# Kernel optimization log

Measured on AMD Instinct MI355X. Metric: run time of the kernel, lower is better.

## Reference

```python
import jax, jax.numpy as jnp
import numpy as np

HIDDEN = 1024
HEADS = 16
HEAD_DIM = HIDDEN // HEADS


def setup_inputs() -> dict:
    key = jax.random.key(0)
    ks = jax.random.split(key, 12)
    B, S, D = 4, 2048, HIDDEN
    scale = 1.0 / np.sqrt(D)
    inp = {
        'q': jax.random.normal(ks[0], (B, S, D), jnp.float32),
        'k': jax.random.normal(ks[1], (B, S, D), jnp.float32),
        'v': jax.random.normal(ks[2], (B, S, D), jnp.float32),
        'Wq': jax.random.normal(ks[3], (D, D), jnp.float32) * scale,
        'bq': jnp.zeros((D,), jnp.float32),
        'Wk': jax.random.normal(ks[4], (D, D), jnp.float32) * scale,
        'bk': jnp.zeros((D,), jnp.float32),
        'Wv': jax.random.normal(ks[5], (D, D), jnp.float32) * scale,
        'bv': jnp.zeros((D,), jnp.float32),
        'Wo': jax.random.normal(ks[6], (D, D), jnp.float32) * scale,
        'bo': jnp.zeros((D,), jnp.float32),
    }
    return inp


def reference(q, k, v, Wq, bq, Wk, bk, Wv, bv, Wo, bo):
    B, S, D = q.shape
    H, Dh = HEADS, HEAD_DIM
    # QKV projections (weights stored as [in, out])
    Q = q @ Wq + bq
    K = k @ Wk + bk
    V = v @ Wv + bv
    # [B, H, S, Dh]
    Qh = Q.reshape(B, S, H, Dh).transpose(0, 2, 1, 3)
    Kh = K.reshape(B, S, H, Dh).transpose(0, 2, 1, 3)
    Vh = V.reshape(B, S, H, Dh).transpose(0, 2, 1, 3)
    # scaled dot-product attention, full [B,H,S,S] scores as in source
    scores = jnp.einsum('bhqd,bhkd->bhqk', Qh, Kh) / jnp.sqrt(jnp.float32(Dh))
    attn = jax.nn.softmax(scores, axis=-1)
    ctx = jnp.einsum('bhqk,bhkd->bhqd', attn, Vh)
    out = ctx.transpose(0, 2, 1, 3).reshape(B, S, D)
    return out @ Wo + bo
```

## Files before the change

### kernel.cpp

```cpp
#include <hip/hip_runtime.h>
#include <hip/hip_bf16.h>

#define HID 1024
#define NH 16
#define DH 64
#define NB 4
#define SQ 2048

typedef __bf16 bf16x8 __attribute__((ext_vector_type(8)));
typedef __bf16 bf16x2 __attribute__((ext_vector_type(2)));
typedef float f32x4 __attribute__((ext_vector_type(4)));
typedef float f32x16 __attribute__((ext_vector_type(16)));
typedef unsigned int u32x4 __attribute__((ext_vector_type(4)));

static __device__ __forceinline__ unsigned pkbf(float a, float b) {
  bf16x2 t; t[0] = (__bf16)a; t[1] = (__bf16)b;
  return __builtin_bit_cast(unsigned, t);
}

static __device__ __forceinline__ void gload16(const void* g, void* l) {
  __builtin_amdgcn_global_load_lds(
      (const __attribute__((address_space(1))) unsigned int*)g,
      (__attribute__((address_space(3))) unsigned int*)l, 16, 0, 0);
}

static __device__ __forceinline__ int xcd_swz(int lin, int nwg) {
  return (lin & 7) * (nwg >> 3) + (lin >> 3);
}

__global__ __launch_bounds__(256) void transpose_wf4_kernel(
    const float* __restrict__ Wq, const float* __restrict__ Wk,
    const float* __restrict__ Wv, const float* __restrict__ Wo,
    __bf16* __restrict__ Wcatf, __bf16* __restrict__ Wof) {
  const int which = blockIdx.z;
  const float* W = which == 0 ? Wq : (which == 1 ? Wk : (which == 2 ? Wv : Wo));
  __bf16* Wf = which == 3 ? Wof : Wcatf + (size_t)which * HID * HID;
  const int nblk = blockIdx.x, kt = blockIdx.y;
  const int tid = threadIdx.x, lane = tid & 63, wid = tid >> 6;
  const int fr = lane & 15, g = lane >> 4;
#pragma unroll
  for (int c = 0; c < 2; ++c) {
    const int wn_i = wid + c * 4;
    const int wn = wn_i >> 2, i = wn_i & 3;
    const int n = nblk * 128 + wn * 64 + i * 16 + fr;
    const int kb = kt * 32 + g * 8;
    bf16x8 v;
#pragma unroll
    for (int e = 0; e < 8; ++e)
      v[e] = (__bf16)W[(size_t)(kb + e) * HID + n];
    *reinterpret_cast<bf16x8*>(
        &Wf[(size_t)(nblk * 32 + kt) * 4096 + wn * 2048 + i * 512 + lane * 8]) = v;
  }
}

__global__ __launch_bounds__(256) void gemm_qkv_kernel(
    const float* __restrict__ Aq, const float* __restrict__ Ak,
    const float* __restrict__ Av, const __bf16* __restrict__ Wcatf,
    const float* __restrict__ bq, const float* __restrict__ bk,
    const float* __restrict__ bv, __bf16* __restrict__ Qh,
    __bf16* __restrict__ Kh, __bf16* __restrict__ Vt, float qscale) {
  const int K = HID;
  __shared__ __align__(16) float Af[2][4096];
  const int tid = threadIdx.x;
  const int lane = tid & 63;
  const int wid = tid >> 6;
  const int wm = wid >> 1, wn = wid & 1;
  const int lin = blockIdx.x + 24 * blockIdx.y;
  const int work = xcd_swz(lin, 1536);
  const int seg = work >> 9;
  const int rem = work & 511;
  const int m0 = (rem >> 3) * 128;
  const int nblk = seg * 8 + (rem & 7);
  const int n0 = nblk * 128;
  const int fr = lane & 15, g = lane >> 4;

  const float* Abase = seg == 0 ? Aq : (seg == 1 ? Ak : Av);
  const int srcswz = ((lane & 7) ^ ((lane >> 3) & 7)) * 4;
  const float* asrc =
      Abase + (size_t)(m0 + wid * 32 + (lane >> 3)) * K + srcswz;
  const __bf16* wsrc = Wcatf + (size_t)nblk * 32 * 4096 + wn * 2048 + lane * 8;

  auto stageA = [&](int buf, int kt) {
    float* ab = &Af[buf][0] + wid * 1024;
#pragma unroll
    for (int j = 0; j < 4; ++j)
      gload16(asrc + (size_t)j * 8 * K + kt * 32, ab + j * 256);
  };
  auto loadB = [&](int kt, bf16x8* br) {
    const __bf16* bp = wsrc + (size_t)kt * 4096;
#pragma unroll
    for (int i = 0; i < 4; ++i)
      br[i] = *reinterpret_cast<const bf16x8*>(bp + i * 512);
  };
  auto readA = [&](int buf, bf16x8* af) {
    const float* ac = &Af[buf][0] + (size_t)wm * 64 * 32;
    const int c0 = ((g * 2) ^ (fr & 7)) * 4;
#pragma unroll
    for (int i = 0; i < 4; ++i) {
      const float* rp = ac + (i * 16 + fr) * 32;
      f32x4 lo = *reinterpret_cast<const f32x4*>(rp + c0);
      f32x4 hi = *reinterpret_cast<const f32x4*>(rp + (c0 ^ 4));
      u32x4 w;
      w[0] = pkbf(lo[0], lo[1]); w[1] = pkbf(lo[2], lo[3]);
      w[2] = pkbf(hi[0], hi[1]); w[3] = pkbf(hi[2], hi[3]);
      af[i] = __builtin_bit_cast(bf16x8, w);
    }
  };

  f32x4 acc[4][4] = {};
  const int NT = K / 32;
  bf16x8 bE[4], bO[4];
  stageA(0, 0);
  loadB(0, bE);
  __syncthreads();
  int cur = 0;
  for (int kt = 0; kt < NT; kt += 2) {
    stageA(cur ^ 1, kt + 1);
    loadB(kt + 1, bO);
    {
      bf16x8 af[4];
      readA(cur, af);
#pragma unroll
      for (int i = 0; i < 4; ++i)
#pragma unroll
        for (int j = 0; j < 4; ++j)
          acc[i][j] = __builtin_amdgcn_mfma_f32_16x16x32_bf16(
              af[i], bE[j], acc[i][j], 0, 0, 0);
    }
    __syncthreads();
    cur ^= 1;
    if (kt + 2 < NT) {
      stageA(cur ^ 1, kt + 2);
      loadB(kt + 2, bE);
    }
    {
      bf16x8 af[4];
      readA(cur, af);
#pragma unroll
      for (int i = 0; i < 4; ++i)
#pragma unroll
        for (int j = 0; j < 4; ++j)
          acc[i][j] = __builtin_amdgcn_mfma_f32_16x16x32_bf16(
              af[i], bO[j], acc[i][j], 0, 0, 0);
    }
    if (kt + 2 < NT) {
      __syncthreads();
      cur ^= 1;
    }
  }

  const float* bias = seg == 0 ? bq : (seg == 1 ? bk : bv);
  const float oscale = seg == 0 ? qscale : 1.f;
#pragma unroll
  for (int i = 0; i < 4; ++i) {
#pragma unroll
    for (int j = 0; j < 4; ++j) {
      const int n = n0 + wn * 64 + j * 16 + fr;
      const int nn = n & 1023;
      const float bn = bias[nn];
      const int h = nn >> 6, dh = nn & (DH - 1);
#pragma unroll
      for (int r = 0; r < 4; ++r) {
        const int m = m0 + wm * 64 + i * 16 + g * 4 + r;
        const float v = (acc[i][j][r] + bn) * oscale;
        const int b = m >> 11, s = m & (SQ - 1);
        if (seg == 0) {
          Qh[(((size_t)(b * NH + h) * SQ) + s) * DH + dh] = (__bf16)v;
        } else if (seg == 1) {
          const int kvt = s >> 5, ql = s & 31;
          const int ds = dh >> 4, hi = (dh >> 3) & 1, e = dh & 7;
          Kh[(size_t)(b * NH + h) * SQ * DH +
             (size_t)kvt * 2048 + ds * 512 + (hi * 32 + ql) * 8 + e] = (__bf16)v;
        } else {
          const int i64 = s >> 6, c16 = (s >> 4) & 3;
          const int hi = (s >> 2) & 1, e = (s & 3) + 4 * ((s >> 3) & 1);
          const int dblk = dh >> 5, ql = dh & 31;
          Vt[(size_t)(b * NH + h) * SQ * DH +
             (size_t)i64 * 4096 + dblk * 2048 + c16 * 512 +
             (hi * 32 + ql) * 8 + e] = (__bf16)v;
        }
      }
    }
  }
}

__global__ __launch_bounds__(256) void gemm_out_kernel(
    const __bf16* __restrict__ Ap, const __bf16* __restrict__ Wof,
    const float* __restrict__ bias, float* __restrict__ out,
    int M, int N, int K) {
  __shared__ __align__(16) char Asm[2][8192];
  const int tid = threadIdx.x;
  const int lane = tid & 63;
  const int wid = tid >> 6;
  const int wm = wid >> 1, wn = wid & 1;
  const int gx = N / 128;
  const int lin = blockIdx.x + gx * blockIdx.y;
  const int work = xcd_swz(lin, gx * (M / 128));
  const int m0 = (work / gx) * 128, nblk = work % gx, n0 = nblk * 128;
  const int fr = lane & 15, g = lane >> 4, kg = (lane >> 4) * 8;

  const __bf16* abf = Ap + (size_t)(m0 + wid * 32 + (lane >> 2)) * K + (lane & 3) * 8;
  const __bf16* wsrc = Wof + (size_t)nblk * 32 * 4096 + wn * 2048 + lane * 8;

  auto stageA = [&](int buf, int kt) {
    char* ab = &Asm[buf][0] + wid * 2048;
#pragma unroll
    for (int j = 0; j < 2; ++j)
      gload16(abf + (size_t)j * 16 * K + kt * 32, ab + j * 1024);
  };
  auto loadB = [&](int kt, bf16x8* br) {
    const __bf16* bp = wsrc + (size_t)kt * 4096;
#pragma unroll
    for (int i = 0; i < 4; ++i)
      br[i] = *reinterpret_cast<const bf16x8*>(bp + i * 512);
  };
  auto readA = [&](int buf, bf16x8* af) {
    const char* ac = &Asm[buf][0];
#pragma unroll
    for (int i = 0; i < 4; ++i)
      af[i] = *reinterpret_cast<const bf16x8*>(
          ac + (wm * 64 + i * 16 + fr) * 64 + kg * 2);
  };

  f32x4 acc[4][4] = {};
  const int NT = K / 32;
  bf16x8 bE[4], bO[4];
  stageA(0, 0);
  loadB(0, bE);
  __syncthreads();
  int cur = 0;
  for (int kt = 0; kt < NT; kt += 2) {
    stageA(cur ^ 1, kt + 1);
    loadB(kt + 1, bO);
    {
      bf16x8 af[4];
      readA(cur, af);
#pragma unroll
      for (int i = 0; i < 4; ++i)
#pragma unroll
        for (int j = 0; j < 4; ++j)
          acc[i][j] = __builtin_amdgcn_mfma_f32_16x16x32_bf16(
              af[i], bE[j], acc[i][j], 0, 0, 0);
    }
    __syncthreads();
    cur ^= 1;
    if (kt + 2 < NT) {
      stageA(cur ^ 1, kt + 2);
      loadB(kt + 2, bE);
    }
    {
      bf16x8 af[4];
      readA(cur, af);
#pragma unroll
      for (int i = 0; i < 4; ++i)
#pragma unroll
        for (int j = 0; j < 4; ++j)
          acc[i][j] = __builtin_amdgcn_mfma_f32_16x16x32_bf16(
              af[i], bO[j], acc[i][j], 0, 0, 0);
    }
    if (kt + 2 < NT) {
      __syncthreads();
      cur ^= 1;
    }
  }

#pragma unroll
  for (int i = 0; i < 4; ++i) {
#pragma unroll
    for (int j = 0; j < 4; ++j) {
      const int n = n0 + wn * 64 + j * 16 + fr;
      const float bn = bias[n];
#pragma unroll
      for (int r = 0; r < 4; ++r) {
        const int m = m0 + wm * 64 + i * 16 + g * 4 + r;
        out[(size_t)m * N + n] = acc[i][j][r] + bn;
      }
    }
  }
}

__global__ __launch_bounds__(256) void attn_kernel(
    const __bf16* __restrict__ Q, const __bf16* __restrict__ K,
    const __bf16* __restrict__ V, __bf16* __restrict__ ctx) {
  __shared__ float tb[4][32][33];
  const int tid = threadIdx.x, lane = tid & 63, wid = tid >> 6;
  const int lin = blockIdx.x + 16 * blockIdx.y;
  const int work = xcd_swz(lin, 16 * NB * NH);
  const int bh = work >> 4;
  const int q0 = (work & 15) * 128 + wid * 32;
  const int ql = lane & 31, hi = lane >> 5;
  const __bf16* Qb = Q + (size_t)bh * SQ * DH;
  const __bf16* Kf = K + (size_t)bh * SQ * DH;
  const __bf16* Vf = V + (size_t)bh * SQ * DH;

  bf16x8 qf[4];
#pragma unroll
  for (int ds = 0; ds < 4; ++ds)
    qf[ds] = *reinterpret_cast<const bf16x8*>(
        &Qb[(size_t)(q0 + ql) * DH + ds * 16 + hi * 8]);

  f32x16 ot0 = {}, ot1 = {};
  float l_run = 0.f;

  for (int kv0 = 0; kv0 < SQ; kv0 += 64) {
    const __bf16* Ka = Kf + (size_t)(kv0 >> 5) * 2048 + lane * 8;
    const __bf16* Kc = Ka + 2048;
    bf16x8 kfa0 = *reinterpret_cast<const bf16x8*>(Ka);
    bf16x8 kfa1 = *reinterpret_cast<const bf16x8*>(Ka + 512);
    bf16x8 kfa2 = *reinterpret_cast<const bf16x8*>(Ka + 1024);
    bf16x8 kfa3 = *reinterpret_cast<const bf16x8*>(Ka + 1536);
    bf16x8 kfb0 = *reinterpret_cast<const bf16x8*>(Kc);
    bf16x8 kfb1 = *reinterpret_cast<const bf16x8*>(Kc + 512);
    bf16x8 kfb2 = *reinterpret_cast<const bf16x8*>(Kc + 1024);
    bf16x8 kfb3 = *reinterpret_cast<const bf16x8*>(Kc + 1536);
    const __bf16* Vbase = Vf + (size_t)(kv0 >> 6) * 4096 + lane * 8;
    bf16x8 v00a = *reinterpret_cast<const bf16x8*>(Vbase);
    bf16x8 v01a = *reinterpret_cast<const bf16x8*>(Vbase + 512);
    bf16x8 v00b = *reinterpret_cast<const bf16x8*>(Vbase + 1024);
    bf16x8 v01b = *reinterpret_cast<const bf16x8*>(Vbase + 1536);
    bf16x8 v10a = *reinterpret_cast<const bf16x8*>(Vbase + 2048);
    bf16x8 v11a = *reinterpret_cast<const bf16x8*>(Vbase + 2560);
    bf16x8 v10b = *reinterpret_cast<const bf16x8*>(Vbase + 3072);
    bf16x8 v11b = *reinterpret_cast<const bf16x8*>(Vbase + 3584);

    f32x16 sa = {}, sb = {};
    __builtin_amdgcn_s_setprio(1);
    sa = __builtin_amdgcn_mfma_f32_32x32x16_bf16(kfa0, qf[0], sa, 0, 0, 0);
    sb = __builtin_amdgcn_mfma_f32_32x32x16_bf16(kfb0, qf[0], sb, 0, 0, 0);
    sa = __builtin_amdgcn_mfma_f32_32x32x16_bf16(kfa1, qf[1], sa, 0, 0, 0);
    sb = __builtin_amdgcn_mfma_f32_32x32x16_bf16(kfb1, qf[1], sb, 0, 0, 0);
    sa = __builtin_amdgcn_mfma_f32_32x32x16_bf16(kfa2, qf[2], sa, 0, 0, 0);
    sb = __builtin_amdgcn_mfma_f32_32x32x16_bf16(kfb2, qf[2], sb, 0, 0, 0);
    sa = __builtin_amdgcn_mfma_f32_32x32x16_bf16(kfa3, qf[3], sa, 0, 0, 0);
    sb = __builtin_amdgcn_mfma_f32_32x32x16_bf16(kfb3, qf[3], sb, 0, 0, 0);
    __builtin_amdgcn_s_setprio(0);

    float pa[16], pb_[16];
#pragma unroll
    for (int r = 0; r < 16; ++r) pa[r] = __builtin_amdgcn_exp2f(sa[r]);
#pragma unroll
    for (int r = 0; r < 16; ++r) pb_[r] = __builtin_amdgcn_exp2f(sb[r]);
    {
      float u0 = 0.f, u1 = 0.f, u2 = 0.f, u3 = 0.f;
#pragma unroll
      for (int r = 0; r < 4; ++r) {
        u0 += pa[r] + pa[r + 4];
        u1 += pa[r + 8] + pa[r + 12];
        u2 += pb_[r] + pb_[r + 4];
        u3 += pb_[r + 8] + pb_[r + 12];
      }
      l_run += (u0 + u1) + (u2 + u3);
    }
    unsigned ca[8], cb[8];
#pragma unroll
    for (int i = 0; i < 8; ++i) {
      ca[i] = pkbf(pa[2 * i], pa[2 * i + 1]);
      cb[i] = pkbf(pb_[2 * i], pb_[2 * i + 1]);
    }
    u32x4 WA0, WA1, WB0, WB1;
    WA0[0] = ca[0]; WA0[1] = ca[1]; WA0[2] = ca[2]; WA0[3] = ca[3];
    WA1[0] = ca[4]; WA1[1] = ca[5]; WA1[2] = ca[6]; WA1[3] = ca[7];
    WB0[0] = cb[0]; WB0[1] = cb[1]; WB0[2] = cb[2]; WB0[3] = cb[3];
    WB1[0] = cb[4]; WB1[1] = cb[5]; WB1[2] = cb[6]; WB1[3] = cb[7];
    bf16x8 pa0 = __builtin_bit_cast(bf16x8, WA0);
    bf16x8 pa1 = __builtin_bit_cast(bf16x8, WA1);
    bf16x8 pb0 = __builtin_bit_cast(bf16x8, WB0);
    bf16x8 pb1 = __builtin_bit_cast(bf16x8, WB1);
    __builtin_amdgcn_s_setprio(1);
    ot0 = __builtin_amdgcn_mfma_f32_32x32x16_bf16(v00a, pa0, ot0, 0, 0, 0);
    ot1 = __builtin_amdgcn_mfma_f32_32x32x16_bf16(v10a, pa0, ot1, 0, 0, 0);
    ot0 = __builtin_amdgcn_mfma_f32_32x32x16_bf16(v01a, pa1, ot0, 0, 0, 0);
    ot1 = __builtin_amdgcn_mfma_f32_32x32x16_bf16(v11a, pa1, ot1, 0, 0, 0);
    ot0 = __builtin_amdgcn_mfma_f32_32x32x16_bf16(v00b, pb0, ot0, 0, 0, 0);
    ot1 = __builtin_amdgcn_mfma_f32_32x32x16_bf16(v10b, pb0, ot1, 0, 0, 0);
    ot0 = __builtin_amdgcn_mfma_f32_32x32x16_bf16(v01b, pb1, ot0, 0, 0, 0);
    ot1 = __builtin_amdgcn_mfma_f32_32x32x16_bf16(v11b, pb1, ot1, 0, 0, 0);
    __builtin_amdgcn_s_setprio(0);
  }
  l_run += __shfl_xor(l_run, 32);
  const float inv = 1.f / l_run;

  const int qr = lane >> 1, hf = lane & 1;
  const int b = bh >> 4, h = bh & 15;
  __bf16* dstb = ctx + ((size_t)(b * SQ + q0 + qr)) * HID + h * 64 + hf * 16;
#pragma unroll
  for (int r = 0; r < 16; ++r)
    tb[wid][ql][(r & 3) + 8 * (r >> 2) + 4 * hi] = ot0[r] * inv;
  {
    unsigned wb[8];
#pragma unroll
    for (int i = 0; i < 8; ++i)
      wb[i] = pkbf(tb[wid][qr][hf * 16 + 2 * i], tb[wid][qr][hf * 16 + 2 * i + 1]);
    u32x4 W0, W1;
    W0[0] = wb[0]; W0[1] = wb[1]; W0[2] = wb[2]; W0[3] = wb[3];
    W1[0] = wb[4]; W1[1] = wb[5]; W1[2] = wb[6]; W1[3] = wb[7];
    *reinterpret_cast<u32x4*>(dstb) = W0;
    *reinterpret_cast<u32x4*>(dstb + 8) = W1;
  }
  __builtin_amdgcn_s_waitcnt(0);
#pragma unroll
  for (int r = 0; r < 16; ++r)
    tb[wid][ql][(r & 3) + 8 * (r >> 2) + 4 * hi] = ot1[r] * inv;
  {
    unsigned wb[8];
#pragma unroll
    for (int i = 0; i < 8; ++i)
      wb[i] = pkbf(tb[wid][qr][hf * 16 + 2 * i], tb[wid][qr][hf * 16 + 2 * i + 1]);
    u32x4 W0, W1;
    W0[0] = wb[0]; W0[1] = wb[1]; W0[2] = wb[2]; W0[3] = wb[3];
    W1[0] = wb[4]; W1[1] = wb[5]; W1[2] = wb[6]; W1[3] = wb[7];
    *reinterpret_cast<u32x4*>(dstb + 32) = W0;
    *reinterpret_cast<u32x4*>(dstb + 40) = W1;
  }
}

extern "C" void kernel_launch(void* const* d_in, const int* in_sizes, int n_in,
                              void* d_out, int out_size, void* d_ws, size_t ws_size,
                              hipStream_t stream) {
  const float* q  = (const float*)d_in[0];
  const float* k  = (const float*)d_in[1];
  const float* v  = (const float*)d_in[2];
  const float* Wq = (const float*)d_in[3];
  const float* bq = (const float*)d_in[4];
  const float* Wk = (const float*)d_in[5];
  const float* bk = (const float*)d_in[6];
  const float* Wv = (const float*)d_in[7];
  const float* bv = (const float*)d_in[8];
  const float* Wo = (const float*)d_in[9];
  const float* bo = (const float*)d_in[10];

  char* ws = (char*)d_ws;
  const size_t WSZ = (size_t)HID * HID * 2;
  const size_t QSZ = (size_t)NB * NH * SQ * DH * 2;
  __bf16* Wcatf = (__bf16*)(ws);
  __bf16* Wof  = (__bf16*)(ws + 3 * WSZ);
  __bf16* Qh   = (__bf16*)(ws + 4 * WSZ);
  __bf16* Kh   = (__bf16*)(ws + 4 * WSZ + QSZ);
  __bf16* Vt   = (__bf16*)(ws + 4 * WSZ + 2 * QSZ);
  __bf16* ctxb = (__bf16*)(ws + 4 * WSZ + 3 * QSZ);

  const int M = NB * SQ;
  const float qscale = 0.125f * 1.44269504088896f;

  transpose_wf4_kernel<<<dim3(8, 32, 4), 256, 0, stream>>>(
      Wq, Wk, Wv, Wo, Wcatf, Wof);

  gemm_qkv_kernel<<<dim3(24, 64), 256, 0, stream>>>(
      q, k, v, Wcatf, bq, bk, bv, Qh, Kh, Vt, qscale);

  attn_kernel<<<dim3(SQ / 128, NB * NH), 256, 0, stream>>>(Qh, Kh, Vt, ctxb);

  gemm_out_kernel<<<dim3(HID / 128, M / 128), 256, 0, stream>>>(
      ctxb, Wof, bo, (float*)d_out, M, HID, HID);
}
```

Measured before the change: 224.4 us.

## Triple-buffer A tiles in QKV GEMM with counted vmcnt waits

Measured after the change: 219.7 us. -2.1%, faster.

```diff
diff --git a/kernel.cpp b/kernel.cpp
--- a/kernel.cpp
+++ b/kernel.cpp
@@ -60,7 +60,7 @@
     const float* __restrict__ bv, __bf16* __restrict__ Qh,
     __bf16* __restrict__ Kh, __bf16* __restrict__ Vt, float qscale) {
   const int K = HID;
-  __shared__ __align__(16) float Af[2][4096];
+  __shared__ __align__(16) float Af[3][4096];
   const int tid = threadIdx.x;
   const int lane = tid & 63;
   const int wid = tid >> 6;
@@ -108,46 +108,42 @@
   };
 
   f32x4 acc[4][4] = {};
-  const int NT = K / 32;
-  bf16x8 bE[4], bO[4];
+  auto mstep = [&](int buf, bf16x8* bR) {
+    bf16x8 af[4];
+    readA(buf, af);
+#pragma unroll
+    for (int i = 0; i < 4; ++i)
+#pragma unroll
+      for (int j = 0; j < 4; ++j)
+        acc[i][j] = __builtin_amdgcn_mfma_f32_16x16x32_bf16(
+            af[i], bR[j], acc[i][j], 0, 0, 0);
+  };
+
+  bf16x8 bP0[4], bP1[4];
   stageA(0, 0);
-  loadB(0, bE);
-  __syncthreads();
-  int cur = 0;
-  for (int kt = 0; kt < NT; kt += 2) {
-    stageA(cur ^ 1, kt + 1);
-    loadB(kt + 1, bO);
-    {
-      bf16x8 af[4];
-      readA(cur, af);
-#pragma unroll
-      for (int i = 0; i < 4; ++i)
-#pragma unroll
-        for (int j = 0; j < 4; ++j)
-          acc[i][j] = __builtin_amdgcn_mfma_f32_16x16x32_bf16(
-              af[i], bE[j], acc[i][j], 0, 0, 0);
-    }
-    __syncthreads();
-    cur ^= 1;
-    if (kt + 2 < NT) {
-      stageA(cur ^ 1, kt + 2);
-      loadB(kt + 2, bE);
-    }
-    {
-      bf16x8 af[4];
-      readA(cur, af);
-#pragma unroll
-      for (int i = 0; i < 4; ++i)
-#pragma unroll
-        for (int j = 0; j < 4; ++j)
-          acc[i][j] = __builtin_amdgcn_mfma_f32_16x16x32_bf16(
-              af[i], bO[j], acc[i][j], 0, 0, 0);
-    }
-    if (kt + 2 < NT) {
-      __syncthreads();
-      cur ^= 1;
-    }
-  }
+  stageA(1, 1);
+  loadB(0, bP0);
+  asm volatile("s_waitcnt vmcnt(8)" ::: "memory");
+  __builtin_amdgcn_s_barrier();
+  __builtin_amdgcn_sched_barrier(0);
+
+  for (int s = 0; s < 30; s += 6) {
+#pragma unroll
+    for (int d = 0; d < 6; ++d) {
+      stageA((d + 2) % 3, s + d + 2);
+      loadB(s + d + 1, (d & 1) ? bP0 : bP1);
+      mstep(d % 3, (d & 1) ? bP1 : bP0);
+      asm volatile("s_waitcnt vmcnt(8)" ::: "memory");
+      __builtin_amdgcn_s_barrier();
+      __builtin_amdgcn_sched_barrier(0);
+    }
+  }
+  loadB(31, bP1);
+  mstep(0, bP0);
+  asm volatile("s_waitcnt vmcnt(4)" ::: "memory");
+  __builtin_amdgcn_s_barrier();
+  __builtin_amdgcn_sched_barrier(0);
+  mstep(1, bP1);
 
   const float* bias = seg == 0 ? bq : (seg == 1 ? bk : bv);
   const float oscale = seg == 0 ? qscale : 1.f;
```
